# Performance work log

Measured on AMD Instinct MI355X. Metric: run time of the kernel, lower is better.

## Reference

```python
import jax, jax.numpy as jnp
from jax import lax
import numpy as np

N_IN = 4          # n_in_channels (WN input); coupling input has 2*N_IN channels
N_CTX = 80        # n_context_channels
N_LAYERS = 8
N_CH = 256        # n_channels (must be even)
K = 3             # kernel_size (odd)
DILATIONS = [1, 2, 4, 8, 16, 32, 64, 128]
B, T = 8, 4096


def conv1d(x, w, b, dilation=1):
    # x: [B, Cin, T], w: [Cout, Cin, K], 'same' padding as in the torch module
    pad = (w.shape[-1] * dilation - dilation) // 2
    y = lax.conv_general_dilated(
        x, w, window_strides=(1,), padding=[(pad, pad)],
        rhs_dilation=(dilation,), dimension_numbers=('NCH', 'OIH', 'NCH'))
    return y + b[None, :, None]


def setup_inputs() -> dict:
    key = jax.random.key(0)
    ks = jax.random.split(key, 14)
    s = 0.05  # weight scale to keep exp(log_s) well-conditioned
    inp = {
        'forecast': jax.random.normal(ks[0], (B, 2 * N_IN, T), jnp.float32),
        'context':  jax.random.normal(ks[1], (B, N_CTX, T), jnp.float32),
        'start_w': jax.random.normal(ks[2], (N_CH, N_IN, 1), jnp.float32) * s,
        'start_b': jax.random.normal(ks[3], (N_CH,), jnp.float32) * s,
        'cond_w':  jax.random.normal(ks[4], (2 * N_CH * N_LAYERS, N_CTX, 1), jnp.float32) * s,
        'cond_b':  jax.random.normal(ks[5], (2 * N_CH * N_LAYERS,), jnp.float32) * s,
        'in_w':    jax.random.normal(ks[6], (N_LAYERS, 2 * N_CH, N_CH, K), jnp.float32) * s,
        'in_b':    jax.random.normal(ks[7], (N_LAYERS, 2 * N_CH), jnp.float32) * s,
        # res_skip: layers 0..L-2 have 2*N_CH out channels; last layer uses only first N_CH
        'rs_w':    jax.random.normal(ks[8], (N_LAYERS, 2 * N_CH, N_CH, 1), jnp.float32) * s,
        'rs_b':    jax.random.normal(ks[9], (N_LAYERS, 2 * N_CH), jnp.float32) * s,
        'end_w':   jax.random.normal(ks[10], (2 * N_IN, N_CH, 1), jnp.float32) * 0.01,
        'end_b':   jax.random.normal(ks[11], (2 * N_IN,), jnp.float32) * 0.01,
    }
    return inp


def wn(f0, context, start_w, start_b, cond_w, cond_b, in_w, in_b, rs_w, rs_b, end_w, end_b):
    x = conv1d(f0, start_w, start_b)                 # [B, N_CH, T]
    ctx = conv1d(context, cond_w, cond_b)            # [B, 2*N_CH*L, T]
    output = jnp.zeros_like(x)
    for i in range(N_LAYERS):
        a = conv1d(x, in_w[i], in_b[i], DILATIONS[i])
        a = a + ctx[:, i * 2 * N_CH:(i + 1) * 2 * N_CH, :]
        acts = jnp.tanh(a[:, :N_CH, :]) * jax.nn.sigmoid(a[:, N_CH:, :])
        if i < N_LAYERS - 1:
            rs = conv1d(acts, rs_w[i], rs_b[i])      # [B, 2*N_CH, T]
            x = x + rs[:, :N_CH, :]
            output = output + rs[:, N_CH:, :]
        else:
            rs = conv1d(acts, rs_w[i][:N_CH], rs_b[i][:N_CH])
            output = output + rs
    return conv1d(output, end_w, end_b)              # [B, 2*N_IN, T]


def reference(forecast, context, start_w, start_b, cond_w, cond_b,
              in_w, in_b, rs_w, rs_b, end_w, end_b):
    n_half = forecast.shape[1] // 2
    f0 = forecast[:, :n_half, :]
    f1 = forecast[:, n_half:, :]
    out = wn(f0, context, start_w, start_b, cond_w, cond_b,
             in_w, in_b, rs_w, rs_b, end_w, end_b)
    log_s = out[:, n_half:, :]
    b = out[:, :n_half, :]
    f1 = jnp.exp(log_s) * f1 + b
    return jnp.concatenate([f0, f1], axis=1), log_s
```

## Files before the change

kernel.cpp:

```cpp
#include <hip/hip_runtime.h>

#define BATCH 8
#define T 4096
#define NCH 256
#define NCTX 80
#define NLAYERS 8

typedef unsigned short u16;
typedef __attribute__((ext_vector_type(8))) short short8;
typedef __attribute__((ext_vector_type(4))) short short4v;
typedef __attribute__((ext_vector_type(4))) float float4v;

__device__ __forceinline__ float b2f(u16 u) {
    unsigned v = ((unsigned)u) << 16;
    float f;
    __builtin_memcpy(&f, &v, 4);
    return f;
}
__device__ __forceinline__ u16 f2b(float f) {
    unsigned v;
    __builtin_memcpy(&v, &f, 4);
    unsigned r = v + 0x7FFFu + ((v >> 16) & 1u);
    return (u16)(r >> 16);
}

typedef const __attribute__((address_space(1))) unsigned int* gp1;
typedef __attribute__((address_space(3))) unsigned int* lp3;
__device__ __forceinline__ void gl_lds16(const u16* g, u16* l) {
    __builtin_amdgcn_global_load_lds((gp1)g, (lp3)l, 16, 0, 0);
}

__device__ __forceinline__ void wb0() { asm volatile("s_waitcnt vmcnt(0) lgkmcnt(0)\n\ts_barrier" ::: "memory"); }
__device__ __forceinline__ void wb4() { asm volatile("s_waitcnt vmcnt(4) lgkmcnt(0)\n\ts_barrier" ::: "memory"); }
__device__ __forceinline__ void wb5() { asm volatile("s_waitcnt vmcnt(5) lgkmcnt(0)\n\ts_barrier" ::: "memory"); }
__device__ __forceinline__ void wb6() { asm volatile("s_waitcnt vmcnt(6) lgkmcnt(0)\n\ts_barrier" ::: "memory"); }
__device__ __forceinline__ void wbn(int n) {
    if (n >= 6) wb6();
    else if (n == 5) wb5();
    else wb4();
}

template <bool F32>
__device__ __forceinline__ float LD(const void* p, size_t i) {
    if constexpr (F32) return ((const float*)p)[i];
    else return b2f(((const u16*)p)[i]);
}
template <bool F32>
__device__ __forceinline__ bool skipv(const int* flag) {
    int f = *flag;
    return F32 ? (f != 0) : (f == 0);
}

__global__ void probe_kernel(const u16* __restrict__ fc, int* __restrict__ flag) {
    __shared__ int cnt;
    if (threadIdx.x == 0) cnt = 0;
    __syncthreads();
    int local = 0;
#pragma unroll
    for (int j = 0; j < 16; j++) {
        u16 u = fc[2 * (threadIdx.x * 16 + j)];
        int e = (u >> 7) & 0xFF;
        if (e >= 0x50 && e <= 0x85) local++;
    }
    atomicAdd(&cnt, local);
    __syncthreads();
    if (threadIdx.x == 0) *flag = (cnt >= 2048) ? 1 : 0;
}

template <bool F32>
__global__ void cvt_kernel(const void* __restrict__ src, u16* __restrict__ dst, int n,
                           const int* __restrict__ flag) {
    if (skipv<F32>(flag)) return;
    int i = blockIdx.x * 256 + threadIdx.x;
    if (i < n) dst[i] = f2b(LD<F32>(src, i));
}

template <bool F32>
__global__ void prep_wc(const void* __restrict__ in_w, const void* __restrict__ in_b,
                        const void* __restrict__ cond_w, const void* __restrict__ cond_b,
                        u16* __restrict__ Wc, const int* __restrict__ flag) {
    if (skipv<F32>(flag)) return;
    int row = blockIdx.x;
    for (int it = 0; it < 4; it++) {
        int col = it * 256 + threadIdx.x;
        if (col >= 864) break;
        float v;
        if (col < 256)       v = LD<F32>(in_w, ((size_t)row * 256 + col) * 3);
        else if (col < 512)  v = LD<F32>(in_w, ((size_t)row * 256 + (col - 256)) * 3 + 1);
        else if (col < 768)  v = LD<F32>(in_w, ((size_t)row * 256 + (col - 512)) * 3 + 2);
        else if (col < 848)  v = LD<F32>(cond_w, (size_t)row * 80 + (col - 768));
        else if (col == 848) v = LD<F32>(in_b, row) + LD<F32>(cond_b, row);
        else                 v = 0.f;
        Wc[(size_t)row * 864 + col] = f2b(v);
    }
}

template <bool F32>
__global__ void prep_ctx(const void* __restrict__ ctx, u16* __restrict__ ctxt,
                         const int* __restrict__ flag) {
    if (skipv<F32>(flag)) return;
    __shared__ float sm[80][65];
    const int tid = threadIdx.x;
    const int b = blockIdx.y, t0 = blockIdx.x * 64;
    for (int it = 0; it < 20; it++) {
        int e = it * 256 + tid;
        int j = e >> 6, tt = e & 63;
        sm[j][tt] = LD<F32>(ctx, ((size_t)b * 80 + j) * T + t0 + tt);
    }
    __syncthreads();
    for (int it = 0; it < 24; it++) {
        int e = it * 256 + tid;
        int r = e / 96, c = e - r * 96;
        float v = (c < 80) ? sm[c][r] : (c == 80 ? 1.f : 0.f);
        ctxt[((size_t)b * T + t0 + r) * 96 + c] = f2b(v);
    }
}

template <bool F32>
__global__ void start_kernel(const void* __restrict__ fc, const void* __restrict__ w,
                             const void* __restrict__ bias, u16* __restrict__ xt,
                             const int* __restrict__ flag) {
    if (skipv<F32>(flag)) return;
    __shared__ float fsm[4][64];
    __shared__ float wsm[1024];
    __shared__ float bsm[256];
    const int tid = threadIdx.x;
    const int b = blockIdx.y, t0 = blockIdx.x * 64;
    fsm[tid >> 6][tid & 63] = LD<F32>(fc, ((size_t)b * 8 + (tid >> 6)) * T + t0 + (tid & 63));
    for (int it = 0; it < 4; it++) wsm[it * 256 + tid] = LD<F32>(w, it * 256 + tid);
    bsm[tid] = LD<F32>(bias, tid);
    __syncthreads();
    for (int r = 0; r < 64; r++) {
        int c = tid;
        float a = bsm[c];
#pragma unroll
        for (int k = 0; k < 4; k++) a += wsm[c * 4 + k] * fsm[k][r];
        xt[((size_t)b * T + t0 + r) * 256 + c] = f2b(a);
    }
}

__global__ __launch_bounds__(256, 2) void layer_conv(
    const u16* __restrict__ x, const u16* __restrict__ Wc, const u16* __restrict__ ctxt,
    u16* __restrict__ acts, int layer, int dil) {
    __shared__ u16 lds[36864];
    const int tid = threadIdx.x;
    const int w = tid >> 6, lane = tid & 63;
    const int l15 = lane & 15, quad = lane >> 4;
    const int iw = w >> 1, jc = w & 1;
    const int b = blockIdx.y;
    const int cblk = blockIdx.x & 1, t0 = (blockIdx.x >> 1) * 128;
    const int lrow = lane >> 2;
    const int fw = (lrow ^ (lrow >> 2)) & 3;
    const int lsw = ((lane & 3) ^ fw) * 8;
    const int fr = (l15 ^ (l15 >> 2)) & 3;
    const int rq = (quad ^ fr) * 8;
    const int brb = 128 * cblk + 64 * (w >> 1) + 256 * (w & 1);

    const u16* xb = x + (size_t)b * T * 256;
    const u16* cb = ctxt + (size_t)b * T * 96;
    const u16* Wl = Wc + (size_t)layer * 512 * 864;

    float4v acc[4][8];
#pragma unroll
    for (int m = 0; m < 4; m++)
#pragma unroll
        for (int jj = 0; jj < 8; jj++) acc[m][jj] = (float4v){0.f, 0.f, 0.f, 0.f};

    auto stageA = [&](int s, int abuf) -> int {
        u16* dst = &lds[abuf * 4096 + w * 512];
        int cnt = 0;
        if (s < 24) {
            int seg = s >> 3, cs = s & 7;
            int tb = t0 + 16 * w + (seg - 1) * dil;
#pragma unroll
            for (int h = 0; h < 2; h++) {
                int tbh = tb + 64 * h;
                u16* d = dst + 2048 * h;
                if (tbh >= 0 && tbh + 16 <= T) {
                    gl_lds16(xb + (size_t)(tbh + lrow) * 256 + cs * 32 + lsw, d);
                    cnt++;
                } else {
                    int t = tbh + lrow;
                    short8 av = (short8){0, 0, 0, 0, 0, 0, 0, 0};
                    if (t >= 0 && t < T)
                        av = *(const short8*)(xb + (size_t)t * 256 + cs * 32 + lsw);
                    *(short4v*)&d[lane * 8] = __builtin_shufflevector(av, av, 0, 1, 2, 3);
                    *(short4v*)&d[lane * 8 + 4] = __builtin_shufflevector(av, av, 4, 5, 6, 7);
                }
            }
        } else {
            gl_lds16(cb + (size_t)(t0 + 16 * w + lrow) * 96 + (s - 24) * 32 + lsw, dst);
            gl_lds16(cb + (size_t)(t0 + 64 + 16 * w + lrow) * 96 + (s - 24) * 32 + lsw, dst + 2048);
            cnt = 2;
        }
        return cnt;
    };
    auto stageB = [&](int s, int bbuf) {
        const u16* src = Wl + (size_t)(brb + lrow) * 864 + s * 32 + lsw;
        u16* dst = &lds[12288 + bbuf * 8192 + w * 2048];
        gl_lds16(src, dst);
        gl_lds16(src + (size_t)16 * 864, dst + 512);
        gl_lds16(src + (size_t)32 * 864, dst + 1024);
        gl_lds16(src + (size_t)48 * 864, dst + 1536);
    };

    int a0 = stageA(0, 0);
    stageB(0, 0);
    int a1 = stageA(1, 1);
    stageB(1, 1);
    (void)a0;
    wbn(4 + a1);
#pragma unroll 1
    for (int s = 0; s < 27; s++) {
        int aiss = 0;
        if (s + 2 < 27) {
            aiss = stageA(s + 2, (s + 2) % 3);
            stageB(s + 2, (s + 2) % 3);
        }
        const u16* bA = &lds[(s % 3) * 4096];
        const u16* bB = &lds[12288 + (s % 3) * 8192];
        short8 af0 = *(const short8*)&bA[(64 * iw + l15) * 32 + rq];
        short8 af1 = *(const short8*)&bA[(64 * iw + 16 + l15) * 32 + rq];
        short8 af2 = *(const short8*)&bA[(64 * iw + 32 + l15) * 32 + rq];
        short8 af3 = *(const short8*)&bA[(64 * iw + 48 + l15) * 32 + rq];
        __builtin_amdgcn_s_setprio(1);
#pragma unroll
        for (int jj = 0; jj < 8; jj++) {
            short8 bf = *(const short8*)&bB[(128 * jc + 16 * jj + l15) * 32 + rq];
            acc[0][jj] = __builtin_amdgcn_mfma_f32_16x16x32_bf16(af0, bf, acc[0][jj], 0, 0, 0);
            acc[1][jj] = __builtin_amdgcn_mfma_f32_16x16x32_bf16(af1, bf, acc[1][jj], 0, 0, 0);
            acc[2][jj] = __builtin_amdgcn_mfma_f32_16x16x32_bf16(af2, bf, acc[2][jj], 0, 0, 0);
            acc[3][jj] = __builtin_amdgcn_mfma_f32_16x16x32_bf16(af3, bf, acc[3][jj], 0, 0, 0);
        }
        __builtin_amdgcn_s_setprio(0);
        if (s < 25) {
            wbn(4 + aiss);
        } else if (s == 25) {
            wb0();
        }
    }

    u16* ab = acts + (size_t)b * T * 256;
#pragma unroll
    for (int m = 0; m < 4; m++)
#pragma unroll
        for (int jj = 0; jj < 4; jj++) {
            int o = 128 * cblk + 64 * jc + 16 * jj + l15;
#pragma unroll
            for (int r = 0; r < 4; r++) {
                int t = t0 + 64 * iw + 16 * m + quad * 4 + r;
                float at = acc[m][jj][r], as = acc[m][jj + 4][r];
                float e2 = __expf(2.f * at);
                float th = 1.f - 2.f / (e2 + 1.f);
                float sg = 1.f / (1.f + __expf(-as));
                ab[(size_t)t * 256 + o] = f2b(th * sg);
            }
        }
}

__global__ __launch_bounds__(256, 2) void layer_rs(
    const u16* __restrict__ acts, u16* __restrict__ x, const u16* __restrict__ Wrs,
    const u16* __restrict__ rsb, u16* __restrict__ oacc, int layer, int first, int last) {
    __shared__ u16 lds[36864];
    const int tid = threadIdx.x;
    const int w = tid >> 6, lane = tid & 63;
    const int l15 = lane & 15, quad = lane >> 4;
    const int iw = w >> 1, jc = w & 1;
    const int b = blockIdx.y;
    const int cblk = blockIdx.x & 1, t0 = (blockIdx.x >> 1) * 128;
    const int lrow = lane >> 2;
    const int fw = (lrow ^ (lrow >> 2)) & 3;
    const int lsw = ((lane & 3) ^ fw) * 8;
    const int fr = (l15 ^ (l15 >> 2)) & 3;
    const int rq = (quad ^ fr) * 8;
    const int brb = 128 * cblk + 64 * (w >> 1) + 256 * (w & 1);

    const u16* ab = acts + (size_t)b * T * 256;
    const u16* Wr = Wrs + (size_t)layer * 512 * 256;

    float4v acc[4][8];
#pragma unroll
    for (int m = 0; m < 4; m++)
#pragma unroll
        for (int jj = 0; jj < 8; jj++) acc[m][jj] = (float4v){0.f, 0.f, 0.f, 0.f};

    auto stageA = [&](int s, int abuf) {
        u16* dst = &lds[abuf * 4096 + w * 512];
        gl_lds16(ab + (size_t)(t0 + 16 * w + lrow) * 256 + s * 32 + lsw, dst);
        gl_lds16(ab + (size_t)(t0 + 64 + 16 * w + lrow) * 256 + s * 32 + lsw, dst + 2048);
    };
    auto stageB = [&](int s, int bbuf) {
        const u16* src = Wr + (size_t)(brb + lrow) * 256 + s * 32 + lsw;
        u16* dst = &lds[12288 + bbuf * 8192 + w * 2048];
        gl_lds16(src, dst);
        gl_lds16(src + (size_t)16 * 256, dst + 512);
        gl_lds16(src + (size_t)32 * 256, dst + 1024);
        gl_lds16(src + (size_t)48 * 256, dst + 1536);
    };

    stageA(0, 0);
    stageB(0, 0);
    stageA(1, 1);
    stageB(1, 1);
    wb6();
#pragma unroll 1
    for (int s = 0; s < 8; s++) {
        if (s + 2 < 8) {
            stageA(s + 2, (s + 2) % 3);
            stageB(s + 2, (s + 2) % 3);
        }
        const u16* bA = &lds[(s % 3) * 4096];
        const u16* bB = &lds[12288 + (s % 3) * 8192];
        short8 af0 = *(const short8*)&bA[(64 * iw + l15) * 32 + rq];
        short8 af1 = *(const short8*)&bA[(64 * iw + 16 + l15) * 32 + rq];
        short8 af2 = *(const short8*)&bA[(64 * iw + 32 + l15) * 32 + rq];
        short8 af3 = *(const short8*)&bA[(64 * iw + 48 + l15) * 32 + rq];
        __builtin_amdgcn_s_setprio(1);
#pragma unroll
        for (int jj = 0; jj < 8; jj++) {
            short8 bf = *(const short8*)&bB[(128 * jc + 16 * jj + l15) * 32 + rq];
            acc[0][jj] = __builtin_amdgcn_mfma_f32_16x16x32_bf16(af0, bf, acc[0][jj], 0, 0, 0);
            acc[1][jj] = __builtin_amdgcn_mfma_f32_16x16x32_bf16(af1, bf, acc[1][jj], 0, 0, 0);
            acc[2][jj] = __builtin_amdgcn_mfma_f32_16x16x32_bf16(af2, bf, acc[2][jj], 0, 0, 0);
            acc[3][jj] = __builtin_amdgcn_mfma_f32_16x16x32_bf16(af3, bf, acc[3][jj], 0, 0, 0);
        }
        __builtin_amdgcn_s_setprio(0);
        if (s < 6) wb6();
        else if (s == 6) wb0();
    }

    u16* xv = x + (size_t)b * T * 256;
    u16* oo = oacc + (size_t)b * T * 256;
#pragma unroll
    for (int m = 0; m < 4; m++)
#pragma unroll
        for (int jj = 0; jj < 8; jj++) {
            int o = 128 * cblk + 64 * jc + 16 * (jj & 3) + l15;
            if (jj < 4) {
                float b0 = b2f(rsb[layer * 512 + o]);
#pragma unroll
                for (int r = 0; r < 4; r++) {
                    int t = t0 + 64 * iw + 16 * m + quad * 4 + r;
                    size_t idx = (size_t)t * 256 + o;
                    float v0 = acc[m][jj][r] + b0;
                    if (last) oo[idx] = f2b(b2f(oo[idx]) + v0);
                    else      xv[idx] = f2b(b2f(xv[idx]) + v0);
                }
            } else if (!last) {
                float b1 = b2f(rsb[layer * 512 + 256 + o]);
#pragma unroll
                for (int r = 0; r < 4; r++) {
                    int t = t0 + 64 * iw + 16 * m + quad * 4 + r;
                    size_t idx = (size_t)t * 256 + o;
                    float v1 = acc[m][jj][r] + b1;
                    oo[idx] = first ? f2b(v1) : f2b(b2f(oo[idx]) + v1);
                }
            }
        }
}

template <bool F32>
__global__ void end_kernel(const u16* __restrict__ oacc, const void* __restrict__ w_end,
                           const void* __restrict__ b_end, const void* __restrict__ fc,
                           void* __restrict__ out, const int* __restrict__ flag) {
    if (skipv<F32>(flag)) return;
    __shared__ float wsm[2048];
    __shared__ float bsm[8];
    const int tid = threadIdx.x;
    for (int it = 0; it < 8; it++) wsm[it * 256 + tid] = LD<F32>(w_end, it * 256 + tid);
    if (tid < 8) bsm[tid] = LD<F32>(b_end, tid);
    __syncthreads();
    int gid = blockIdx.x * 256 + tid;
    int b = gid >> 12, t = gid & 4095;
    float o8[8];
#pragma unroll
    for (int o = 0; o < 8; o++) o8[o] = bsm[o];
    const u16* orow = oacc + (size_t)(b * T + t) * 256;
    for (int c8 = 0; c8 < 32; c8++) {
        short8 v8 = *(const short8*)(orow + c8 * 8);
#pragma unroll
        for (int k = 0; k < 8; k++) {
            float v = b2f((u16)v8[k]);
            int c = c8 * 8 + k;
#pragma unroll
            for (int o = 0; o < 8; o++) o8[o] += wsm[o * 256 + c] * v;
        }
    }
    size_t ob8 = (size_t)b * 8 * T;
#pragma unroll
    for (int j = 0; j < 4; j++) {
        float f1v = LD<F32>(fc, ob8 + (size_t)(4 + j) * T + t);
        float ls = o8[4 + j];
        float val = __expf(ls) * f1v + o8[j];
        if constexpr (F32) {
            float* o = (float*)out;
            o[ob8 + (size_t)j * T + t] = ((const float*)fc)[ob8 + (size_t)j * T + t];
            o[ob8 + (size_t)(4 + j) * T + t] = val;
            o[(size_t)BATCH * 8 * T + ((size_t)b * 4 + j) * T + t] = ls;
        } else {
            u16* o = (u16*)out;
            o[ob8 + (size_t)j * T + t] = ((const u16*)fc)[ob8 + (size_t)j * T + t];
            o[ob8 + (size_t)(4 + j) * T + t] = f2b(val);
            o[(size_t)BATCH * 8 * T + ((size_t)b * 4 + j) * T + t] = f2b(ls);
        }
    }
}

template <bool F32>
static void launch_prep(const void* forecast, const void* context, const void* start_w,
                        const void* start_b, const void* cond_w, const void* cond_b,
                        const void* in_w, const void* in_b, const void* rs_w, const void* rs_b,
                        u16* xA, u16* ctxt, u16* Wc, u16* Wrs, u16* rsb, const int* flag,
                        hipStream_t stream) {
    cvt_kernel<F32><<<4096, 256, 0, stream>>>(rs_w, Wrs, 8 * 512 * 256, flag);
    cvt_kernel<F32><<<16, 256, 0, stream>>>(rs_b, rsb, 4096, flag);
    prep_wc<F32><<<4096, 256, 0, stream>>>(in_w, in_b, cond_w, cond_b, Wc, flag);
    prep_ctx<F32><<<dim3(64, BATCH), 256, 0, stream>>>(context, ctxt, flag);
    start_kernel<F32><<<dim3(64, BATCH), 256, 0, stream>>>(forecast, start_w, start_b, xA, flag);
}

extern "C" void kernel_launch(void* const* d_in, const int* in_sizes, int n_in,
                              void* d_out, int out_size, void* d_ws, size_t ws_size,
                              hipStream_t stream) {
    const void* forecast = d_in[0];
    const void* context  = d_in[1];
    const void* start_w  = d_in[2];
    const void* start_b  = d_in[3];
    const void* cond_w   = d_in[4];
    const void* cond_b   = d_in[5];
    const void* in_w     = d_in[6];
    const void* in_b     = d_in[7];
    const void* rs_w     = d_in[8];
    const void* rs_b     = d_in[9];
    const void* end_w    = d_in[10];
    const void* end_b    = d_in[11];

    char* W = (char*)d_ws;
    int* flag = (int*)(W + 0);
    u16* xA   = (u16*)(W + 256);
    u16* oacc = (u16*)(W + 256 + 16777216);
    u16* acts = (u16*)(W + 256 + 33554432);
    u16* ctxt = (u16*)(W + 256 + 50331648);
    u16* Wc   = (u16*)(W + 256 + 56623104);
    u16* Wrs  = (u16*)(W + 256 + 63700992);
    u16* rsb  = (u16*)(W + 256 + 65798144);

    probe_kernel<<<1, 256, 0, stream>>>((const u16*)forecast, flag);

    launch_prep<false>(forecast, context, start_w, start_b, cond_w, cond_b, in_w, in_b, rs_w,
                       rs_b, xA, ctxt, Wc, Wrs, rsb, flag, stream);
    launch_prep<true>(forecast, context, start_w, start_b, cond_w, cond_b, in_w, in_b, rs_w,
                      rs_b, xA, ctxt, Wc, Wrs, rsb, flag, stream);

    const int dil[NLAYERS] = {1, 2, 4, 8, 16, 32, 64, 128};
    for (int l = 0; l < NLAYERS; l++) {
        layer_conv<<<dim3(64, BATCH), 256, 0, stream>>>(xA, Wc, ctxt, acts, l, dil[l]);
        layer_rs<<<dim3(64, BATCH), 256, 0, stream>>>(acts, xA, Wrs, rsb, oacc, l,
                                                      l == 0, l == NLAYERS - 1);
    }

    end_kernel<false><<<128, 256, 0, stream>>>(oacc, end_w, end_b, forecast, d_out, flag);
    end_kernel<true><<<128, 256, 0, stream>>>(oacc, end_w, end_b, forecast, d_out, flag);
}
```

Measured before the change: 709.1 us.

## Load A operand fragments directly from global into registers, bypassing LDS

In both layer_conv and layer_rs, the activation (A) operand is no longer staged through LDS with a triple buffer. Each lane now loads its MFMA fragments straight from global memory into registers, one step ahead, and only the weights keep going through LDS. This removes the A-tile LDS writes and reads, drops the boundary-fallback copy path, and shrinks shared memory from 72KB to 48KB. In exchange, the A prefetch is issued only after the current MFMAs, so its global latency sits almost directly before the next step's use. Rows shared between the two column waves are also fetched twice from global or cache.

```diff
diff --git a/kernel.cpp b/kernel.cpp
--- a/kernel.cpp
+++ b/kernel.cpp
@@ -32,13 +32,7 @@
 
 __device__ __forceinline__ void wb0() { asm volatile("s_waitcnt vmcnt(0) lgkmcnt(0)\n\ts_barrier" ::: "memory"); }
 __device__ __forceinline__ void wb4() { asm volatile("s_waitcnt vmcnt(4) lgkmcnt(0)\n\ts_barrier" ::: "memory"); }
-__device__ __forceinline__ void wb5() { asm volatile("s_waitcnt vmcnt(5) lgkmcnt(0)\n\ts_barrier" ::: "memory"); }
-__device__ __forceinline__ void wb6() { asm volatile("s_waitcnt vmcnt(6) lgkmcnt(0)\n\ts_barrier" ::: "memory"); }
-__device__ __forceinline__ void wbn(int n) {
-    if (n >= 6) wb6();
-    else if (n == 5) wb5();
-    else wb4();
-}
+__device__ __forceinline__ void wb8() { asm volatile("s_waitcnt vmcnt(8) lgkmcnt(0)\n\ts_barrier" ::: "memory"); }
 
 template <bool F32>
 __device__ __forceinline__ float LD(const void* p, size_t i) {
@@ -142,7 +136,7 @@
 __global__ __launch_bounds__(256, 2) void layer_conv(
     const u16* __restrict__ x, const u16* __restrict__ Wc, const u16* __restrict__ ctxt,
     u16* __restrict__ acts, int layer, int dil) {
-    __shared__ u16 lds[36864];
+    __shared__ u16 lds[24576];
     const int tid = threadIdx.x;
     const int w = tid >> 6, lane = tid & 63;
     const int l15 = lane & 15, quad = lane >> 4;
@@ -166,78 +160,59 @@
 #pragma unroll
         for (int jj = 0; jj < 8; jj++) acc[m][jj] = (float4v){0.f, 0.f, 0.f, 0.f};
 
-    auto stageA = [&](int s, int abuf) -> int {
-        u16* dst = &lds[abuf * 4096 + w * 512];
-        int cnt = 0;
+    short8 afc[4];
+
+    auto loadA = [&](int s) {
         if (s < 24) {
             int seg = s >> 3, cs = s & 7;
-            int tb = t0 + 16 * w + (seg - 1) * dil;
-#pragma unroll
-            for (int h = 0; h < 2; h++) {
-                int tbh = tb + 64 * h;
-                u16* d = dst + 2048 * h;
-                if (tbh >= 0 && tbh + 16 <= T) {
-                    gl_lds16(xb + (size_t)(tbh + lrow) * 256 + cs * 32 + lsw, d);
-                    cnt++;
-                } else {
-                    int t = tbh + lrow;
-                    short8 av = (short8){0, 0, 0, 0, 0, 0, 0, 0};
-                    if (t >= 0 && t < T)
-                        av = *(const short8*)(xb + (size_t)t * 256 + cs * 32 + lsw);
-                    *(short4v*)&d[lane * 8] = __builtin_shufflevector(av, av, 0, 1, 2, 3);
-                    *(short4v*)&d[lane * 8 + 4] = __builtin_shufflevector(av, av, 4, 5, 6, 7);
-                }
+            int off = cs * 32 + quad * 8;
+            int tb = t0 + 64 * iw + l15 + (seg - 1) * dil;
+#pragma unroll
+            for (int m = 0; m < 4; m++) {
+                int tr = tb + 16 * m;
+                int trc = tr < 0 ? 0 : (tr > T - 1 ? T - 1 : tr);
+                short8 v = *(const short8*)(xb + (size_t)trc * 256 + off);
+                if (tr < 0 || tr >= T) v = (short8){0, 0, 0, 0, 0, 0, 0, 0};
+                afc[m] = v;
             }
         } else {
-            gl_lds16(cb + (size_t)(t0 + 16 * w + lrow) * 96 + (s - 24) * 32 + lsw, dst);
-            gl_lds16(cb + (size_t)(t0 + 64 + 16 * w + lrow) * 96 + (s - 24) * 32 + lsw, dst + 2048);
-            cnt = 2;
-        }
-        return cnt;
+            int off = (s - 24) * 32 + quad * 8;
+            int tb = t0 + 64 * iw + l15;
+#pragma unroll
+            for (int m = 0; m < 4; m++)
+                afc[m] = *(const short8*)(cb + (size_t)(tb + 16 * m) * 96 + off);
+        }
     };
     auto stageB = [&](int s, int bbuf) {
         const u16* src = Wl + (size_t)(brb + lrow) * 864 + s * 32 + lsw;
-        u16* dst = &lds[12288 + bbuf * 8192 + w * 2048];
+        u16* dst = &lds[bbuf * 8192 + w * 2048];
         gl_lds16(src, dst);
         gl_lds16(src + (size_t)16 * 864, dst + 512);
         gl_lds16(src + (size_t)32 * 864, dst + 1024);
         gl_lds16(src + (size_t)48 * 864, dst + 1536);
     };
 
-    int a0 = stageA(0, 0);
+    loadA(0);
     stageB(0, 0);
-    int a1 = stageA(1, 1);
     stageB(1, 1);
-    (void)a0;
-    wbn(4 + a1);
+    wb4();
 #pragma unroll 1
     for (int s = 0; s < 27; s++) {
-        int aiss = 0;
-        if (s + 2 < 27) {
-            aiss = stageA(s + 2, (s + 2) % 3);
-            stageB(s + 2, (s + 2) % 3);
-        }
-        const u16* bA = &lds[(s % 3) * 4096];
-        const u16* bB = &lds[12288 + (s % 3) * 8192];
-        short8 af0 = *(const short8*)&bA[(64 * iw + l15) * 32 + rq];
-        short8 af1 = *(const short8*)&bA[(64 * iw + 16 + l15) * 32 + rq];
-        short8 af2 = *(const short8*)&bA[(64 * iw + 32 + l15) * 32 + rq];
-        short8 af3 = *(const short8*)&bA[(64 * iw + 48 + l15) * 32 + rq];
+        if (s + 2 < 27) stageB(s + 2, (s + 2) % 3);
+        const u16* bB = &lds[(s % 3) * 8192];
         __builtin_amdgcn_s_setprio(1);
 #pragma unroll
         for (int jj = 0; jj < 8; jj++) {
             short8 bf = *(const short8*)&bB[(128 * jc + 16 * jj + l15) * 32 + rq];
-            acc[0][jj] = __builtin_amdgcn_mfma_f32_16x16x32_bf16(af0, bf, acc[0][jj], 0, 0, 0);
-            acc[1][jj] = __builtin_amdgcn_mfma_f32_16x16x32_bf16(af1, bf, acc[1][jj], 0, 0, 0);
-            acc[2][jj] = __builtin_amdgcn_mfma_f32_16x16x32_bf16(af2, bf, acc[2][jj], 0, 0, 0);
-            acc[3][jj] = __builtin_amdgcn_mfma_f32_16x16x32_bf16(af3, bf, acc[3][jj], 0, 0, 0);
+            acc[0][jj] = __builtin_amdgcn_mfma_f32_16x16x32_bf16(afc[0], bf, acc[0][jj], 0, 0, 0);
+            acc[1][jj] = __builtin_amdgcn_mfma_f32_16x16x32_bf16(afc[1], bf, acc[1][jj], 0, 0, 0);
+            acc[2][jj] = __builtin_amdgcn_mfma_f32_16x16x32_bf16(afc[2], bf, acc[2][jj], 0, 0, 0);
+            acc[3][jj] = __builtin_amdgcn_mfma_f32_16x16x32_bf16(afc[3], bf, acc[3][jj], 0, 0, 0);
         }
         __builtin_amdgcn_s_setprio(0);
-        if (s < 25) {
-            wbn(4 + aiss);
-        } else if (s == 25) {
-            wb0();
-        }
+        if (s + 1 < 27) loadA(s + 1);
+        if (s < 25) wb8();
+        else if (s == 25) wb4();
     }
 
     u16* ab = acts + (size_t)b * T * 256;
@@ -261,7 +236,7 @@
 __global__ __launch_bounds__(256, 2) void layer_rs(
     const u16* __restrict__ acts, u16* __restrict__ x, const u16* __restrict__ Wrs,
     const u16* __restrict__ rsb, u16* __restrict__ oacc, int layer, int first, int last) {
-    __shared__ u16 lds[36864];
+    __shared__ u16 lds[24576];
     const int tid = threadIdx.x;
     const int w = tid >> 6, lane = tid & 63;
     const int l15 = lane & 15, quad = lane >> 4;
@@ -284,49 +259,44 @@
 #pragma unroll
         for (int jj = 0; jj < 8; jj++) acc[m][jj] = (float4v){0.f, 0.f, 0.f, 0.f};
 
-    auto stageA = [&](int s, int abuf) {
-        u16* dst = &lds[abuf * 4096 + w * 512];
-        gl_lds16(ab + (size_t)(t0 + 16 * w + lrow) * 256 + s * 32 + lsw, dst);
-        gl_lds16(ab + (size_t)(t0 + 64 + 16 * w + lrow) * 256 + s * 32 + lsw, dst + 2048);
+    short8 afc[4];
+    auto loadA = [&](int s) {
+        int off = s * 32 + quad * 8;
+        int tb = t0 + 64 * iw + l15;
+#pragma unroll
+        for (int m = 0; m < 4; m++)
+            afc[m] = *(const short8*)(ab + (size_t)(tb + 16 * m) * 256 + off);
     };
     auto stageB = [&](int s, int bbuf) {
         const u16* src = Wr + (size_t)(brb + lrow) * 256 + s * 32 + lsw;
-        u16* dst = &lds[12288 + bbuf * 8192 + w * 2048];
+        u16* dst = &lds[bbuf * 8192 + w * 2048];
         gl_lds16(src, dst);
         gl_lds16(src + (size_t)16 * 256, dst + 512);
         gl_lds16(src + (size_t)32 * 256, dst + 1024);
         gl_lds16(src + (size_t)48 * 256, dst + 1536);
     };
 
-    stageA(0, 0);
+    loadA(0);
     stageB(0, 0);
-    stageA(1, 1);
     stageB(1, 1);
-    wb6();
+    wb4();
 #pragma unroll 1
     for (int s = 0; s < 8; s++) {
-        if (s + 2 < 8) {
-            stageA(s + 2, (s + 2) % 3);
-            stageB(s + 2, (s + 2) % 3);
-        }
-        const u16* bA = &lds[(s % 3) * 4096];
-        const u16* bB = &lds[12288 + (s % 3) * 8192];
-        short8 af0 = *(const short8*)&bA[(64 * iw + l15) * 32 + rq];
-        short8 af1 = *(const short8*)&bA[(64 * iw + 16 + l15) * 32 + rq];
-        short8 af2 = *(const short8*)&bA[(64 * iw + 32 + l15) * 32 + rq];
-        short8 af3 = *(const short8*)&bA[(64 * iw + 48 + l15) * 32 + rq];
+        if (s + 2 < 8) stageB(s + 2, (s + 2) % 3);
+        const u16* bB = &lds[(s % 3) * 8192];
         __builtin_amdgcn_s_setprio(1);
 #pragma unroll
         for (int jj = 0; jj < 8; jj++) {
             short8 bf = *(const short8*)&bB[(128 * jc + 16 * jj + l15) * 32 + rq];
-            acc[0][jj] = __builtin_amdgcn_mfma_f32_16x16x32_bf16(af0, bf, acc[0][jj], 0, 0, 0);
-            acc[1][jj] = __builtin_amdgcn_mfma_f32_16x16x32_bf16(af1, bf, acc[1][jj], 0, 0, 0);
-            acc[2][jj] = __builtin_amdgcn_mfma_f32_16x16x32_bf16(af2, bf, acc[2][jj], 0, 0, 0);
-            acc[3][jj] = __builtin_amdgcn_mfma_f32_16x16x32_bf16(af3, bf, acc[3][jj], 0, 0, 0);
+            acc[0][jj] = __builtin_amdgcn_mfma_f32_16x16x32_bf16(afc[0], bf, acc[0][jj], 0, 0, 0);
+            acc[1][jj] = __builtin_amdgcn_mfma_f32_16x16x32_bf16(afc[1], bf, acc[1][jj], 0, 0, 0);
+            acc[2][jj] = __builtin_amdgcn_mfma_f32_16x16x32_bf16(afc[2], bf, acc[2][jj], 0, 0, 0);
+            acc[3][jj] = __builtin_amdgcn_mfma_f32_16x16x32_bf16(afc[3], bf, acc[3][jj], 0, 0, 0);
         }
         __builtin_amdgcn_s_setprio(0);
-        if (s < 6) wb6();
-        else if (s == 6) wb0();
+        if (s + 1 < 8) loadA(s + 1);
+        if (s < 6) wb8();
+        else if (s == 6) wb4();
     }
 
     u16* xv = x + (size_t)b * T * 256;
```

Result: slower. 845.6 us (+19.2%).
